# Optimization experiments

Measured on AMD Instinct MI355X. Metric: run time of the kernel, lower is better.

Reference implementation:

```python
import jax, jax.numpy as jnp
import numpy as np

HIDDEN = 1024
HORIZON = 24
BATCH, SEQ, D_IN = 256, 512, 64


def setup_inputs() -> dict:
    key = jax.random.key(0)
    k1, k2, k3, k4, k5 = jax.random.split(key, 5)
    fan_in = D_IN + HIDDEN
    # flax Dense default: lecun_normal kernel, zero bias; use scaled normal
    W = jax.random.normal(k1, (fan_in, 4 * HIDDEN), jnp.float32) / np.sqrt(fan_in)
    b = jnp.zeros((4 * HIDDEN,), jnp.float32)
    Wout = jax.random.normal(k2, (HIDDEN, HORIZON), jnp.float32) / np.sqrt(HIDDEN)
    bout = jnp.zeros((HORIZON,), jnp.float32)
    x = jax.random.normal(k3, (BATCH, SEQ, D_IN), jnp.float32)
    return {"x": x, "W": W, "b": b, "Wout": Wout, "bout": bout}


def reference(x, W, b, Wout, bout):
    B, T, D = x.shape
    H = W.shape[1] // 4

    def step(carry, x_t):
        h, c = carry
        gates = jnp.concatenate([x_t, h], axis=-1) @ W + b  # [B, 4H]
        i, f, g, o = jnp.split(gates, 4, axis=-1)
        i = jax.nn.sigmoid(i)
        f = jax.nn.sigmoid(f)
        o = jax.nn.sigmoid(o)
        g = jnp.tanh(g)
        c = f * c + i * g
        h = o * jnp.tanh(c)
        return (h, c), None

    init = (jnp.zeros((B, H), x.dtype), jnp.zeros((B, H), x.dtype))
    (h_final, _), _ = jax.lax.scan(step, init, jnp.swapaxes(x, 0, 1))
    return h_final @ Wout + bout  # [B, horizon]
```

## Files before the change

kernel.cpp:

```cpp
#include <hip/hip_runtime.h>
#include <hip/hip_fp16.h>


#define T_STEPS 512
#define HID 1024
#define GRID 256
#define NTHR 512

typedef __attribute__((ext_vector_type(8))) _Float16 half8;
typedef __attribute__((ext_vector_type(4))) float f32x4;
typedef __attribute__((ext_vector_type(2))) float f32x2;

__device__ __forceinline__ float sigm(float v) {
    return __builtin_amdgcn_rcpf(1.0f + __expf(-v));
}
__device__ __forceinline__ float tanh_fast(float v) {
    return 2.0f * __builtin_amdgcn_rcpf(1.0f + __expf(-2.0f * v)) - 1.0f;
}

__global__ void pack_w(const float* __restrict__ W, _Float16* __restrict__ Wp) {
    int idx = blockIdx.x * 256 + threadIdx.x;
    const int total = 64 * 136 * 64;
    if (idx >= total) return;
    int col = idx & 63;
    int kb = (idx >> 6) % 136;
    int n = (idx >> 6) / 136;
    int oc = ((col & 3) << 10) + (n << 4) + (col >> 2);
    const float* src = W + (size_t)(kb * 8) * 4096 + oc;
    _Float16* dst = Wp + (size_t)idx * 8;
#pragma unroll
    for (int j = 0; j < 8; j++) dst[j] = (_Float16)src[(size_t)j * 4096];
}

__global__ void __launch_bounds__(NTHR, 2) lstm_persist(
    const float* __restrict__ x,
    const _Float16* __restrict__ Wp,
    const float* __restrict__ bias,
    _Float16* __restrict__ hbuf,
    float* __restrict__ hfinal,
    unsigned int* bar)
{
    __shared__ float P[4 * 64 * 64];
    _Float16* hstage = (_Float16*)P;

    int wg = blockIdx.x;
    int xcd = wg & 7, slot = wg >> 3;
    int n = (xcd << 3) + (slot & 7);
    int m = slot >> 3;
    int B0 = m << 6;

    int tid = threadIdx.x;
    int wave = tid >> 6;
    int lane = tid & 63;
    int l15 = lane & 15, l4 = lane >> 4;
    int bb = tid & 63;
    int u0 = tid >> 6;

    float breg[2][4];
#pragma unroll
    for (int q = 0; q < 2; q++) {
        int u = (u0 << 1) + q;
#pragma unroll
        for (int g = 0; g < 4; g++) breg[q][g] = bias[(g << 10) + (n << 4) + u];
    }

    float cst[2] = {0.f, 0.f};

    const size_t HB = (size_t)128 * 256 * 8;
    const _Float16* WpBase = Wp + (size_t)n * 136 * 64 * 8;

    half8 wfr[4][4];
#pragma unroll
    for (int j = 0; j < 4; j++) {
        int kb = ((2 + wave + 8 * j) << 2) + l4;
        const _Float16* wp = WpBase + ((size_t)kb << 9);
#pragma unroll
        for (int nn = 0; nn < 4; nn++) wfr[j][nn] = *(const half8*)(wp + (((nn << 4) + l15) << 3));
    }

    half8 bxr[4];
    if (wave == 2 || wave == 3) {
        int kb = ((wave - 2) << 2) + l4;
        const _Float16* wp = WpBase + ((size_t)kb << 9);
#pragma unroll
        for (int nn = 0; nn < 4; nn++) bxr[nn] = *(const half8*)(wp + (((nn << 4) + l15) << 3));
    }

    f32x4 acc[4][4];
#pragma unroll
    for (int i = 0; i < 4; i++)
#pragma unroll
        for (int j = 0; j < 4; j++) acc[i][j] = (f32x4){0.f, 0.f, 0.f, 0.f};

    auto XPREP = [&](int tt) {
        if (wave == 2 || wave == 3) {
            int kb = ((wave - 2) << 2) + l4;
#pragma unroll
            for (int mm = 0; mm < 4; mm++) {
                const float* xp = x + ((size_t)(B0 + (mm << 4) + l15) * T_STEPS + tt) * 64 + (kb << 3);
                f32x4 lo = *(const f32x4*)xp;
                f32x4 hi = *(const f32x4*)(xp + 4);
                half8 v;
                v[0] = (_Float16)lo[0]; v[1] = (_Float16)lo[1];
                v[2] = (_Float16)lo[2]; v[3] = (_Float16)lo[3];
                v[4] = (_Float16)hi[0]; v[5] = (_Float16)hi[1];
                v[6] = (_Float16)hi[2]; v[7] = (_Float16)hi[3];
#pragma unroll
                for (int nn = 0; nn < 4; nn++)
                    acc[mm][nn] = __builtin_amdgcn_mfma_f32_16x16x32_f16(v, bxr[nn], acc[mm][nn], 0, 0, 0);
            }
        }
    };

    XPREP(0);

    for (int t = 0; t < T_STEPS; t++) {
        const _Float16* cur = hbuf + (size_t)(t & 1) * HB;
        _Float16* nxt = hbuf + (size_t)((t + 1) & 1) * HB;

#pragma unroll
        for (int j = 0; j < 4; j++) {
            int kb = ((2 + wave + 8 * j) << 2) + l4;
            unsigned long long* hp =
                (unsigned long long*)(cur + (((size_t)(kb - 8) << 8) + B0 + l15) * 8);
            half8 ah[4];
#pragma unroll
            for (int mm = 0; mm < 4; mm++) {
                union { unsigned long long u[2]; half8 h; } cv;
                cv.u[0] = __hip_atomic_load(hp + (mm << 5), __ATOMIC_RELAXED, __HIP_MEMORY_SCOPE_AGENT);
                cv.u[1] = __hip_atomic_load(hp + (mm << 5) + 1, __ATOMIC_RELAXED, __HIP_MEMORY_SCOPE_AGENT);
                ah[mm] = cv.h;
            }
#pragma unroll
            for (int mm = 0; mm < 4; mm++)
#pragma unroll
                for (int nn = 0; nn < 4; nn++)
                    acc[mm][nn] = __builtin_amdgcn_mfma_f32_16x16x32_f16(ah[mm], wfr[j][nn],
                                                                         acc[mm][nn], 0, 0, 0);
        }

        if (wave < 4) {
#pragma unroll
            for (int mm = 0; mm < 4; mm++)
#pragma unroll
                for (int nn = 0; nn < 4; nn++) {
                    int c = (nn << 4) + l15;
                    int bblk = (mm << 2) + l4;
                    int word = (((wave << 6) + c) << 6) + (((bblk ^ l15) & 15) << 2);
                    *(f32x4*)&P[word] = acc[mm][nn];
                }
        }
        __syncthreads();
        if (wave >= 4) {
            int pw = wave - 4;
#pragma unroll
            for (int mm = 0; mm < 4; mm++)
#pragma unroll
                for (int nn = 0; nn < 4; nn++) {
                    int c = (nn << 4) + l15;
                    int bblk = (mm << 2) + l4;
                    int word = (((pw << 6) + c) << 6) + (((bblk ^ l15) & 15) << 2);
                    f32x4 v = *(f32x4*)&P[word];
                    v += acc[mm][nn];
                    *(f32x4*)&P[word] = v;
                }
        }
        __syncthreads();

        union { _Float16 h2[2]; unsigned int u; } hs;
        float hvf[2];
#pragma unroll
        for (int q = 0; q < 2; q++) {
            int u = (u0 << 1) + q;
            float g4[4];
#pragma unroll
            for (int g = 0; g < 4; g++) {
                int c = (u << 2) + g;
                int word = (c << 6) + (((((bb >> 2) ^ c) & 15) << 2) | (bb & 3));
                float s = breg[q][g];
#pragma unroll
                for (int w = 0; w < 4; w++) s += P[(w << 12) + word];
                g4[g] = s;
            }
            float ig = sigm(g4[0]);
            float fg = sigm(g4[1]);
            float gg = tanh_fast(g4[2]);
            float og = sigm(g4[3]);
            float cv = fg * cst[q] + ig * gg;
            cst[q] = cv;
            float hv = og * tanh_fast(cv);
            hs.h2[q] = (_Float16)hv;
            hvf[q] = hv;
        }
        if (t == T_STEPS - 1) {
            int ug0 = (n << 4) + (u0 << 1);
            f32x2 hv2; hv2[0] = hvf[0]; hv2[1] = hvf[1];
            *(f32x2*)&hfinal[(size_t)(B0 + bb) * HID + ug0] = hv2;
            break;
        }

        __syncthreads();
        *(unsigned int*)&hstage[(bb << 4) + (u0 << 1)] = hs.u;
        __syncthreads();

        if (wave == 0) {
#pragma unroll
            for (int it = 0; it < 2; it++) {
                int item = lane + (it << 6);
                int row = item >> 1, hf = item & 1;
                union { half8 h; unsigned long long u[2]; } v;
                v.h = *(const half8*)&hstage[(row << 4) + (hf << 3)];
                unsigned long long* dst =
                    (unsigned long long*)(nxt + (((size_t)((n << 1) + hf) << 8) + B0 + row) * 8);
                __hip_atomic_store(dst, v.u[0], __ATOMIC_RELAXED, __HIP_MEMORY_SCOPE_AGENT);
                __hip_atomic_store(dst + 1, v.u[1], __ATOMIC_RELAXED, __HIP_MEMORY_SCOPE_AGENT);
            }
            asm volatile("s_waitcnt vmcnt(0)" ::: "memory");
            if (lane == 0)
                __hip_atomic_store(bar + (wg << 4), (unsigned int)(t + 1), __ATOMIC_RELAXED,
                                   __HIP_MEMORY_SCOPE_AGENT);
        }

#pragma unroll
        for (int i = 0; i < 4; i++)
#pragma unroll
            for (int j = 0; j < 4; j++) acc[i][j] = (f32x4){0.f, 0.f, 0.f, 0.f};
        XPREP(t + 1);
        if (tid >= 256 && tid < 320) {
            const unsigned int* ap = bar + (((m << 6) + (tid - 256)) << 4);
            while (__hip_atomic_load(ap, __ATOMIC_RELAXED, __HIP_MEMORY_SCOPE_AGENT) <
                   (unsigned int)(t + 1)) {
                __builtin_amdgcn_s_sleep(1);
            }
        }
        __syncthreads();
    }
}

__global__ void proj_kernel(const float* __restrict__ hfinal, const float* __restrict__ Wout,
                            const float* __restrict__ bout, float* __restrict__ out) {
    int b = blockIdx.x;
    int l = threadIdx.x;
    float acc[24];
#pragma unroll
    for (int j = 0; j < 24; j++) acc[j] = 0.f;
    for (int i = 0; i < 16; i++) {
        int k = i * 64 + l;
        float h = hfinal[(size_t)b * HID + k];
        const float* wr = Wout + (size_t)k * 24;
#pragma unroll
        for (int j = 0; j < 24; j++) acc[j] += h * wr[j];
    }
    __shared__ float red[24][65];
#pragma unroll
    for (int j = 0; j < 24; j++) red[j][l] = acc[j];
    __syncthreads();
    if (l < 24) {
        float s = bout[l];
#pragma unroll
        for (int i = 0; i < 64; i++) s += red[l][i];
        out[b * 24 + l] = s;
    }
}

extern "C" void kernel_launch(void* const* d_in, const int* in_sizes, int n_in,
                              void* d_out, int out_size, void* d_ws, size_t ws_size,
                              hipStream_t stream) {
    const float* x = (const float*)d_in[0];
    const float* W = (const float*)d_in[1];
    const float* b = (const float*)d_in[2];
    const float* Wout = (const float*)d_in[3];
    const float* bout = (const float*)d_in[4];
    float* out = (float*)d_out;

    char* ws = (char*)d_ws;
    _Float16* Wp = (_Float16*)ws;
    _Float16* hbuf = (_Float16*)(ws + 8912896);
    float* hfinal = (float*)(ws + 8912896 + 1048576);
    unsigned int* bar = (unsigned int*)(ws + 8912896 + 2097152);

    hipMemsetAsync(hbuf, 0, (size_t)128 * 256 * 8 * sizeof(_Float16), stream);
    hipMemsetAsync(bar, 0, 16384, stream);

    pack_w<<<(64 * 136 * 64 + 255) / 256, 256, 0, stream>>>(W, Wp);

    void* args[6];
    args[0] = (void*)&x;
    args[1] = (void*)&Wp;
    args[2] = (void*)&b;
    args[3] = (void*)&hbuf;
    args[4] = (void*)&hfinal;
    args[5] = (void*)&bar;
    hipLaunchCooperativeKernel((void*)lstm_persist, dim3(GRID), dim3(NTHR), args, 0, stream);

    proj_kernel<<<256, 64, 0, stream>>>(hfinal, Wout, bout, out);
}
```

Before: 3.492 ms.

## Split each workgroup's batch tile into two half-tiles with staggered barrier phases

Each workgroup's 64-row batch tile is split into two 32-row halves processed in alternating phases, each with its own barrier counter array. While one half's h update propagates across workgroups, the other half computes, so the grid-wide barrier latency is meant to overlap with useful MFMA work. The trade-off is twice as many syncthreads and barrier polls per step and smaller MFMA batches per phase. The LDS reduction buffer is halved and the barrier memset is doubled to match.

```diff
diff --git a/kernel.cpp b/kernel.cpp
--- a/kernel.cpp
+++ b/kernel.cpp
@@ -9,7 +9,7 @@
 
 typedef __attribute__((ext_vector_type(8))) _Float16 half8;
 typedef __attribute__((ext_vector_type(4))) float f32x4;
-typedef __attribute__((ext_vector_type(2))) float f32x2;
+typedef unsigned long long u64;
 
 __device__ __forceinline__ float sigm(float v) {
     return __builtin_amdgcn_rcpf(1.0f + __expf(-v));
@@ -40,7 +40,7 @@
     float* __restrict__ hfinal,
     unsigned int* bar)
 {
-    __shared__ float P[4 * 64 * 64];
+    __shared__ float P[4 * 64 * 32];
     _Float16* hstage = (_Float16*)P;
 
     int wg = blockIdx.x;
@@ -53,18 +53,14 @@
     int wave = tid >> 6;
     int lane = tid & 63;
     int l15 = lane & 15, l4 = lane >> 4;
-    int bb = tid & 63;
-    int u0 = tid >> 6;
-
-    float breg[2][4];
-#pragma unroll
-    for (int q = 0; q < 2; q++) {
-        int u = (u0 << 1) + q;
-#pragma unroll
-        for (int g = 0; g < 4; g++) breg[q][g] = bias[(g << 10) + (n << 4) + u];
-    }
-
-    float cst[2] = {0.f, 0.f};
+    int r_ = tid & 31;
+    int u_ = tid >> 5;
+
+    float breg_[4];
+#pragma unroll
+    for (int g = 0; g < 4; g++) breg_[g] = bias[(g << 10) + (n << 4) + u_];
+
+    float cstA = 0.f, cstB = 0.f;
 
     const size_t HB = (size_t)128 * 256 * 8;
     const _Float16* WpBase = Wp + (size_t)n * 136 * 64 * 8;
@@ -77,7 +73,6 @@
 #pragma unroll
         for (int nn = 0; nn < 4; nn++) wfr[j][nn] = *(const half8*)(wp + (((nn << 4) + l15) << 3));
     }
-
     half8 bxr[4];
     if (wave == 2 || wave == 3) {
         int kb = ((wave - 2) << 2) + l4;
@@ -86,18 +81,22 @@
         for (int nn = 0; nn < 4; nn++) bxr[nn] = *(const half8*)(wp + (((nn << 4) + l15) << 3));
     }
 
-    f32x4 acc[4][4];
-#pragma unroll
-    for (int i = 0; i < 4; i++)
-#pragma unroll
-        for (int j = 0; j < 4; j++) acc[i][j] = (f32x4){0.f, 0.f, 0.f, 0.f};
-
-    auto XPREP = [&](int tt) {
+    auto PHASE = [&](int c, float& cst, int t, int pollC, int pollT) {
+        const _Float16* cur = hbuf + (size_t)(t & 1) * HB;
+        _Float16* nxt = hbuf + (size_t)((t + 1) & 1) * HB;
+        int B0c = B0 + (c << 5);
+
+        f32x4 acc[2][4];
+#pragma unroll
+        for (int i = 0; i < 2; i++)
+#pragma unroll
+            for (int j = 0; j < 4; j++) acc[i][j] = (f32x4){0.f, 0.f, 0.f, 0.f};
+
         if (wave == 2 || wave == 3) {
             int kb = ((wave - 2) << 2) + l4;
 #pragma unroll
-            for (int mm = 0; mm < 4; mm++) {
-                const float* xp = x + ((size_t)(B0 + (mm << 4) + l15) * T_STEPS + tt) * 64 + (kb << 3);
+            for (int mm = 0; mm < 2; mm++) {
+                const float* xp = x + ((size_t)(B0c + (mm << 4) + l15) * T_STEPS + t) * 64 + (kb << 3);
                 f32x4 lo = *(const f32x4*)xp;
                 f32x4 hi = *(const f32x4*)(xp + 4);
                 half8 v;
@@ -110,29 +109,21 @@
                     acc[mm][nn] = __builtin_amdgcn_mfma_f32_16x16x32_f16(v, bxr[nn], acc[mm][nn], 0, 0, 0);
             }
         }
-    };
-
-    XPREP(0);
-
-    for (int t = 0; t < T_STEPS; t++) {
-        const _Float16* cur = hbuf + (size_t)(t & 1) * HB;
-        _Float16* nxt = hbuf + (size_t)((t + 1) & 1) * HB;
 
 #pragma unroll
         for (int j = 0; j < 4; j++) {
             int kb = ((2 + wave + 8 * j) << 2) + l4;
-            unsigned long long* hp =
-                (unsigned long long*)(cur + (((size_t)(kb - 8) << 8) + B0 + l15) * 8);
-            half8 ah[4];
-#pragma unroll
-            for (int mm = 0; mm < 4; mm++) {
-                union { unsigned long long u[2]; half8 h; } cv;
+            u64* hp = (u64*)(cur + (((size_t)(kb - 8) << 8) + B0c + l15) * 8);
+            half8 ah[2];
+#pragma unroll
+            for (int mm = 0; mm < 2; mm++) {
+                union { u64 u[2]; half8 h; } cv;
                 cv.u[0] = __hip_atomic_load(hp + (mm << 5), __ATOMIC_RELAXED, __HIP_MEMORY_SCOPE_AGENT);
                 cv.u[1] = __hip_atomic_load(hp + (mm << 5) + 1, __ATOMIC_RELAXED, __HIP_MEMORY_SCOPE_AGENT);
                 ah[mm] = cv.h;
             }
 #pragma unroll
-            for (int mm = 0; mm < 4; mm++)
+            for (int mm = 0; mm < 2; mm++)
 #pragma unroll
                 for (int nn = 0; nn < 4; nn++)
                     acc[mm][nn] = __builtin_amdgcn_mfma_f32_16x16x32_f16(ah[mm], wfr[j][nn],
@@ -141,25 +132,24 @@
 
         if (wave < 4) {
 #pragma unroll
-            for (int mm = 0; mm < 4; mm++)
+            for (int mm = 0; mm < 2; mm++)
 #pragma unroll
                 for (int nn = 0; nn < 4; nn++) {
-                    int c = (nn << 4) + l15;
-                    int bblk = (mm << 2) + l4;
-                    int word = (((wave << 6) + c) << 6) + (((bblk ^ l15) & 15) << 2);
+                    int cc = (nn << 4) + l15;
+                    int rblk = (mm << 2) + l4;
+                    int word = (wave << 11) + (cc << 5) + (((rblk ^ (cc & 7)) & 7) << 2);
                     *(f32x4*)&P[word] = acc[mm][nn];
                 }
         }
         __syncthreads();
         if (wave >= 4) {
-            int pw = wave - 4;
-#pragma unroll
-            for (int mm = 0; mm < 4; mm++)
+#pragma unroll
+            for (int mm = 0; mm < 2; mm++)
 #pragma unroll
                 for (int nn = 0; nn < 4; nn++) {
-                    int c = (nn << 4) + l15;
-                    int bblk = (mm << 2) + l4;
-                    int word = (((pw << 6) + c) << 6) + (((bblk ^ l15) & 15) << 2);
+                    int cc = (nn << 4) + l15;
+                    int rblk = (mm << 2) + l4;
+                    int word = ((wave - 4) << 11) + (cc << 5) + (((rblk ^ (cc & 7)) & 7) << 2);
                     f32x4 v = *(f32x4*)&P[word];
                     v += acc[mm][nn];
                     *(f32x4*)&P[word] = v;
@@ -167,73 +157,57 @@
         }
         __syncthreads();
 
-        union { _Float16 h2[2]; unsigned int u; } hs;
-        float hvf[2];
-#pragma unroll
-        for (int q = 0; q < 2; q++) {
-            int u = (u0 << 1) + q;
-            float g4[4];
-#pragma unroll
-            for (int g = 0; g < 4; g++) {
-                int c = (u << 2) + g;
-                int word = (c << 6) + (((((bb >> 2) ^ c) & 15) << 2) | (bb & 3));
-                float s = breg[q][g];
-#pragma unroll
-                for (int w = 0; w < 4; w++) s += P[(w << 12) + word];
-                g4[g] = s;
-            }
-            float ig = sigm(g4[0]);
-            float fg = sigm(g4[1]);
-            float gg = tanh_fast(g4[2]);
-            float og = sigm(g4[3]);
-            float cv = fg * cst[q] + ig * gg;
-            cst[q] = cv;
-            float hv = og * tanh_fast(cv);
-            hs.h2[q] = (_Float16)hv;
-            hvf[q] = hv;
-        }
+        float g4[4];
+#pragma unroll
+        for (int g = 0; g < 4; g++) {
+            int cc = (u_ << 2) + g;
+            int word = (cc << 5) + ((((r_ >> 2) ^ (cc & 7)) & 7) << 2) + (r_ & 3);
+            float s = breg_[g];
+#pragma unroll
+            for (int w = 0; w < 4; w++) s += P[(w << 11) + word];
+            g4[g] = s;
+        }
+        float ig = sigm(g4[0]);
+        float fg = sigm(g4[1]);
+        float gg = tanh_fast(g4[2]);
+        float og = sigm(g4[3]);
+        float cv = fg * cst + ig * gg;
+        cst = cv;
+        float hv = og * tanh_fast(cv);
+
         if (t == T_STEPS - 1) {
-            int ug0 = (n << 4) + (u0 << 1);
-            f32x2 hv2; hv2[0] = hvf[0]; hv2[1] = hvf[1];
-            *(f32x2*)&hfinal[(size_t)(B0 + bb) * HID + ug0] = hv2;
-            break;
-        }
-
-        __syncthreads();
-        *(unsigned int*)&hstage[(bb << 4) + (u0 << 1)] = hs.u;
-        __syncthreads();
-
-        if (wave == 0) {
-#pragma unroll
-            for (int it = 0; it < 2; it++) {
-                int item = lane + (it << 6);
-                int row = item >> 1, hf = item & 1;
-                union { half8 h; unsigned long long u[2]; } v;
+            hfinal[(size_t)(B0c + r_) * HID + (n << 4) + u_] = hv;
+        } else {
+            __syncthreads();
+            hstage[(r_ << 4) + u_] = (_Float16)hv;
+            __syncthreads();
+            if (wave == 0) {
+                int row = lane >> 1, hf = lane & 1;
+                union { half8 h; u64 u[2]; } v;
                 v.h = *(const half8*)&hstage[(row << 4) + (hf << 3)];
-                unsigned long long* dst =
-                    (unsigned long long*)(nxt + (((size_t)((n << 1) + hf) << 8) + B0 + row) * 8);
+                u64* dst = (u64*)(nxt + (((size_t)((n << 1) + hf) << 8) + B0c + row) * 8);
                 __hip_atomic_store(dst, v.u[0], __ATOMIC_RELAXED, __HIP_MEMORY_SCOPE_AGENT);
                 __hip_atomic_store(dst + 1, v.u[1], __ATOMIC_RELAXED, __HIP_MEMORY_SCOPE_AGENT);
-            }
-            asm volatile("s_waitcnt vmcnt(0)" ::: "memory");
-            if (lane == 0)
-                __hip_atomic_store(bar + (wg << 4), (unsigned int)(t + 1), __ATOMIC_RELAXED,
-                                   __HIP_MEMORY_SCOPE_AGENT);
-        }
-
-#pragma unroll
-        for (int i = 0; i < 4; i++)
-#pragma unroll
-            for (int j = 0; j < 4; j++) acc[i][j] = (f32x4){0.f, 0.f, 0.f, 0.f};
-        XPREP(t + 1);
-        if (tid >= 256 && tid < 320) {
-            const unsigned int* ap = bar + (((m << 6) + (tid - 256)) << 4);
+                asm volatile("s_waitcnt vmcnt(0)" ::: "memory");
+                if (lane == 0)
+                    __hip_atomic_store(bar + (((c << 8) + wg) << 4), (unsigned int)(t + 1),
+                                       __ATOMIC_RELAXED, __HIP_MEMORY_SCOPE_AGENT);
+            }
+        }
+
+        if (pollT >= 0 && tid >= 256 && tid < 320) {
+            const unsigned int* ap = bar + (((pollC << 8) + (m << 6) + (tid - 256)) << 4);
             while (__hip_atomic_load(ap, __ATOMIC_RELAXED, __HIP_MEMORY_SCOPE_AGENT) <
-                   (unsigned int)(t + 1)) {
+                   (unsigned int)pollT) {
                 __builtin_amdgcn_s_sleep(1);
             }
         }
         __syncthreads();
+    };
+
+    for (int t = 0; t < T_STEPS; t++) {
+        PHASE(0, cstA, t, 1, t);
+        PHASE(1, cstB, t, 0, (t < T_STEPS - 1) ? (t + 1) : -1);
     }
 }
 
@@ -279,8 +253,8 @@
     float* hfinal = (float*)(ws + 8912896 + 1048576);
     unsigned int* bar = (unsigned int*)(ws + 8912896 + 2097152);
 
-    hipMemsetAsync(hbuf, 0, (size_t)128 * 256 * 8 * sizeof(_Float16), stream);
-    hipMemsetAsync(bar, 0, 16384, stream);
+    hipMemsetAsync(hbuf, 0, 524288, stream);
+    hipMemsetAsync(bar, 0, 32768, stream);
 
     pack_w<<<(64 * 136 * 64 + 255) / 256, 256, 0, stream>>>(W, Wp);
 
```

New measurement: 3.613 ms. +3.5%, slower.
